# Kernel optimization log

Hardware: AMD Instinct MI355X
Metric: run time of the kernel (lower is better)

Reference implementation:

```python
import jax, jax.numpy as jnp
import numpy as np

EPS_NORM = 1e-12   # F.normalize clamp
EPS_DIV = 1e-6


def _l2_normalize(x):
    n = jnp.linalg.norm(x, axis=-1, keepdims=True)
    return x / jnp.maximum(n, EPS_NORM)


def _sync_stats(video, audio):
    # video, audio: [B, L]
    L = video.shape[-1]
    v = _l2_normalize(video)
    a = _l2_normalize(audio)
    # full cross-correlation per sample -> [B, 2L-1] (same as np.correlate mode='full')
    corr = jax.vmap(lambda vi, ai: jnp.correlate(vi, ai, mode='full'))(v, a)
    peak_idx = jnp.argmax(corr, axis=-1)                     # [B]
    delay = (peak_idx - (L - 1)).astype(jnp.float32)         # center = (2L-1)//2 = L-1
    vnorm = jnp.linalg.norm(v, axis=-1)
    anorm = jnp.linalg.norm(a, axis=-1)
    corr_strength = jnp.max(corr, axis=-1) / (vnorm * anorm + EPS_DIV)
    corr_variance = jnp.std(corr, axis=-1)
    video_energy = jnp.sum(v * v, axis=-1)
    audio_energy = jnp.sum(a * a, axis=-1)
    energy_ratio = video_energy / (audio_energy + EPS_DIV)
    d = v - a
    # |mean(exp(i d))| without complex dtype
    phase_coherence = jnp.sqrt(jnp.mean(jnp.cos(d), axis=-1) ** 2
                               + jnp.mean(jnp.sin(d), axis=-1) ** 2)
    consistency = 1.0 / (1.0 + jnp.abs(delay))
    return jnp.stack([delay / 10.0, corr_strength, corr_variance,
                      energy_ratio, phase_coherence, consistency], axis=-1)  # [B, 6]


def setup_inputs() -> dict:
    key = jax.random.key(0)
    k1, k2, k3, k4, k5, k6 = jax.random.split(key, 6)
    B, L, F = 65536, 128, 32
    return {
        'video_features': jax.random.normal(k1, (B, L), dtype=jnp.float32),
        'audio_features': jax.random.normal(k2, (B, L), dtype=jnp.float32),
        'W1': jax.random.normal(k3, (6, 16), dtype=jnp.float32) * 0.3,
        'b1': jax.random.normal(k4, (16,), dtype=jnp.float32) * 0.1,
        'W2': jax.random.normal(k5, (16, F), dtype=jnp.float32) * 0.2,
        'b2': jax.random.normal(k6, (F,), dtype=jnp.float32) * 0.1,
    }


def reference(video_features, audio_features, W1, b1, W2, b2):
    s = _sync_stats(video_features, audio_features)          # [B, 6]
    h = jax.nn.relu(s @ W1 + b1)                              # [B, 16]
    return h @ W2 + b2                                        # [B, 32]
```

## Files before the change

kernel.cpp:

```cpp
#include <hip/hip_runtime.h>

#define NEG_BIG (-3.0e38f)

__device__ __forceinline__ int swz(int s) { return s ^ ((s >> 3) & 7); }

__global__ __launch_bounds__(256) void avsync_kernel(
    const float* __restrict__ video, const float* __restrict__ audio,
    const float* __restrict__ W1, const float* __restrict__ b1,
    const float* __restrict__ W2, const float* __restrict__ b2,
    float* __restrict__ out) {
  __shared__ float lds[4][2][512];

  const int tid  = threadIdx.x;
  const int wid  = tid >> 6;
  const int lane = tid & 63;
  const int half = lane >> 5;
  const int m    = lane & 31;
  const int b    = (int)blockIdx.x * 8 + wid * 2 + half;

  float* ap  = &lds[wid][half][0];
  float* vl  = &lds[wid][half][384];
  char*  apc = reinterpret_cast<char*>(ap);

  const float4 vr = *reinterpret_cast<const float4*>(video + (size_t)b * 128 + 4 * m);
  const float4 ar = *reinterpret_cast<const float4*>(audio + (size_t)b * 128 + 4 * m);

  float4 z4; z4.x = z4.y = z4.z = z4.w = 0.0f;
  *reinterpret_cast<float4*>(apc + (swz(m)      << 4)) = z4;
  *reinterpret_cast<float4*>(apc + (swz(32 + m) << 4)) = ar;
  *reinterpret_cast<float4*>(apc + (swz(64 + m) << 4)) = z4;
  reinterpret_cast<float4*>(vl)[m] = vr;

  float pv = vr.x * vr.x + vr.y * vr.y + vr.z * vr.z + vr.w * vr.w;
  float pa = ar.x * ar.x + ar.y * ar.y + ar.z * ar.z + ar.w * ar.w;
#pragma unroll
  for (int off = 1; off < 32; off <<= 1) {
    pv += __shfl_xor(pv, off, 32);
    pa += __shfl_xor(pa, off, 32);
  }
  const float nv = sqrtf(pv);
  const float na = sqrtf(pa);
  const float iv = 1.0f / fmaxf(nv, 1e-12f);
  const float ia = 1.0f / fmaxf(na, 1e-12f);

  const float d0 = vr.x * iv - ar.x * ia;
  const float d1 = vr.y * iv - ar.y * ia;
  const float d2 = vr.z * iv - ar.z * ia;
  const float d3 = vr.w * iv - ar.w * ia;
  float sc = __cosf(d0) + __cosf(d1) + __cosf(d2) + __cosf(d3);
  float ss = __sinf(d0) + __sinf(d1) + __sinf(d2) + __sinf(d3);
#pragma unroll
  for (int off = 1; off < 32; off <<= 1) {
    sc += __shfl_xor(sc, off, 32);
    ss += __shfl_xor(ss, off, 32);
  }

  float W[12];
  {
    const float4 t0 = *reinterpret_cast<const float4*>(apc + (swz(2 * m)     << 4));
    const float4 t1 = *reinterpret_cast<const float4*>(apc + (swz(2 * m + 1) << 4));
    const float4 t2 = *reinterpret_cast<const float4*>(apc + (swz(2 * m + 2) << 4));
    W[0] = t0.x; W[1] = t0.y; W[2]  = t0.z; W[3]  = t0.w;
    W[4] = t1.x; W[5] = t1.y; W[6]  = t1.z; W[7]  = t1.w;
    W[8] = t2.x; W[9] = t2.y; W[10] = t2.z; W[11] = t2.w;
  }
  const float4* vlp = reinterpret_cast<const float4*>(vl);
  float acc[8] = {0.f, 0.f, 0.f, 0.f, 0.f, 0.f, 0.f, 0.f};
#pragma unroll
  for (int c = 0; c < 32; ++c) {
    const float4 v4 = vlp[c];
#pragma unroll
    for (int q = 0; q < 8; ++q) {
      acc[q] = fmaf(v4.x, W[7 - q],  acc[q]);
      acc[q] = fmaf(v4.y, W[8 - q],  acc[q]);
      acc[q] = fmaf(v4.z, W[9 - q],  acc[q]);
      acc[q] = fmaf(v4.w, W[10 - q], acc[q]);
    }
    if (c < 31) {
      const float4 tn = *reinterpret_cast<const float4*>(apc + (swz(2 * m + 3 + c) << 4));
#pragma unroll
      for (int k = 0; k < 8; ++k) W[k] = W[k + 4];
      W[8] = tn.x; W[9] = tn.y; W[10] = tn.z; W[11] = tn.w;
    }
  }

  const int sh0 = 248 - 8 * m;
  float sum = 0.f, ssq = 0.f, mx = NEG_BIG;
  int mi = 0;
#pragma unroll
  for (int q = 0; q < 8; ++q) {
    const int sh = sh0 + q;
    const bool realLag = (sh < 255);
    const float cv = acc[q];
    const float cs = realLag ? cv : 0.f;
    sum += cs;
    ssq += cs * cs;
    const float cm = realLag ? cv : NEG_BIG;
    if (cm > mx) { mx = cm; mi = sh; }
  }
#pragma unroll
  for (int off = 1; off < 32; off <<= 1) {
    const float ov = __shfl_xor(mx, off, 32);
    const int   oi = __shfl_xor(mi, off, 32);
    if (ov > mx || (ov == mx && oi < mi)) { mx = ov; mi = oi; }
    sum += __shfl_xor(sum, off, 32);
    ssq += __shfl_xor(ssq, off, 32);
  }

  const float s = iv * ia;
  const float delay = (float)mi - 127.0f;
  const float rv = nv / fmaxf(nv, 1e-12f);
  const float ra = na / fmaxf(na, 1e-12f);
  const float cstr = (mx * s) / (rv * ra + 1e-6f);
  const float mean_r = sum * (1.0f / 255.0f);
  const float var_r  = fmaxf(ssq * (1.0f / 255.0f) - mean_r * mean_r, 0.0f);
  const float cstd = s * sqrtf(var_r);
  const float ve = rv * rv, ae = ra * ra;
  const float er = ve / (ae + 1e-6f);
  const float mc = sc * (1.0f / 128.0f), ms = ss * (1.0f / 128.0f);
  const float pc = sqrtf(mc * mc + ms * ms);
  const float cons = 1.0f / (1.0f + fabsf(delay));

  const float s0 = delay * 0.1f;
  const float s1 = cstr;
  const float s2 = cstd;
  const float s3 = er;
  const float s4 = pc;
  const float s5 = cons;

  float h[16];
#pragma unroll
  for (int k = 0; k < 16; ++k) {
    float acch = b1[k];
    acch = fmaf(s0, W1[0 * 16 + k], acch);
    acch = fmaf(s1, W1[1 * 16 + k], acch);
    acch = fmaf(s2, W1[2 * 16 + k], acch);
    acch = fmaf(s3, W1[3 * 16 + k], acch);
    acch = fmaf(s4, W1[4 * 16 + k], acch);
    acch = fmaf(s5, W1[5 * 16 + k], acch);
    h[k] = fmaxf(acch, 0.0f);
  }
  float o = b2[m];
#pragma unroll
  for (int k = 0; k < 16; ++k) o = fmaf(h[k], W2[k * 32 + m], o);
  out[(size_t)b * 32 + m] = o;
}

extern "C" void kernel_launch(void* const* d_in, const int* in_sizes, int n_in,
                              void* d_out, int out_size, void* d_ws, size_t ws_size,
                              hipStream_t stream) {
  const float* video = (const float*)d_in[0];
  const float* audio = (const float*)d_in[1];
  const float* W1 = (const float*)d_in[2];
  const float* b1 = (const float*)d_in[3];
  const float* W2 = (const float*)d_in[4];
  const float* b2 = (const float*)d_in[5];
  float* out = (float*)d_out;

  const int B = in_sizes[0] / 128;
  const int blocks = B / 8;
  avsync_kernel<<<blocks, 256, 0, stream>>>(video, audio, W1, b1, W2, b2, out);
}
```

Before: 88.67 us.

## Restructure cross-correlation lag mapping with rotating register window and unswizzled LDS

Each lane now computes two groups of four lags (4m..4m+3 and 128+4m..) instead of eight contiguous lags. The shifted audio windows are read as float4 from an unswizzled, padded LDS buffer using a three-register rotation, with loads prefetched one chunk ahead. The change also sets launch_bounds to 8 blocks per unit and drops the XOR swizzle. The aim is to cut register shuffling and LDS address arithmetic and to raise occupancy, at the risk of LDS bank conflicts from the unswizzled reads and register pressure under the new bound.

```diff
diff --git a/kernel.cpp b/kernel.cpp
--- a/kernel.cpp
+++ b/kernel.cpp
@@ -2,14 +2,12 @@
 
 #define NEG_BIG (-3.0e38f)
 
-__device__ __forceinline__ int swz(int s) { return s ^ ((s >> 3) & 7); }
-
-__global__ __launch_bounds__(256) void avsync_kernel(
+__global__ __launch_bounds__(256, 8) void avsync_kernel(
     const float* __restrict__ video, const float* __restrict__ audio,
     const float* __restrict__ W1, const float* __restrict__ b1,
     const float* __restrict__ W2, const float* __restrict__ b2,
     float* __restrict__ out) {
-  __shared__ float lds[4][2][512];
+  __shared__ float lds[4][2][544];
 
   const int tid  = threadIdx.x;
   const int wid  = tid >> 6;
@@ -18,21 +16,21 @@
   const int m    = lane & 31;
   const int b    = (int)blockIdx.x * 8 + wid * 2 + half;
 
-  float* ap  = &lds[wid][half][0];
-  float* vl  = &lds[wid][half][384];
-  char*  apc = reinterpret_cast<char*>(ap);
-
-  const float4 vr = *reinterpret_cast<const float4*>(video + (size_t)b * 128 + 4 * m);
-  const float4 ar = *reinterpret_cast<const float4*>(audio + (size_t)b * 128 + 4 * m);
+  float* hbase = &lds[wid][half][0];
+
+  const float4 v4 = *reinterpret_cast<const float4*>(video + (size_t)b * 128 + 4 * m);
+  const float4 a4 = *reinterpret_cast<const float4*>(audio + (size_t)b * 128 + 4 * m);
 
   float4 z4; z4.x = z4.y = z4.z = z4.w = 0.0f;
-  *reinterpret_cast<float4*>(apc + (swz(m)      << 4)) = z4;
-  *reinterpret_cast<float4*>(apc + (swz(32 + m) << 4)) = ar;
-  *reinterpret_cast<float4*>(apc + (swz(64 + m) << 4)) = z4;
-  reinterpret_cast<float4*>(vl)[m] = vr;
-
-  float pv = vr.x * vr.x + vr.y * vr.y + vr.z * vr.z + vr.w * vr.w;
-  float pa = ar.x * ar.x + ar.y * ar.y + ar.z * ar.z + ar.w * ar.w;
+  float4* sl = reinterpret_cast<float4*>(hbase);
+  sl[m]      = z4;
+  sl[64 + m] = z4;
+  if (m < 2) sl[96 + m] = z4;
+  sl[32 + m] = a4;
+  *reinterpret_cast<float4*>(hbase + 392 + 4 * m) = v4;
+
+  float pv = v4.x * v4.x + v4.y * v4.y + v4.z * v4.z + v4.w * v4.w;
+  float pa = a4.x * a4.x + a4.y * a4.y + a4.z * a4.z + a4.w * a4.w;
 #pragma unroll
   for (int off = 1; off < 32; off <<= 1) {
     pv += __shfl_xor(pv, off, 32);
@@ -43,10 +41,10 @@
   const float iv = 1.0f / fmaxf(nv, 1e-12f);
   const float ia = 1.0f / fmaxf(na, 1e-12f);
 
-  const float d0 = vr.x * iv - ar.x * ia;
-  const float d1 = vr.y * iv - ar.y * ia;
-  const float d2 = vr.z * iv - ar.z * ia;
-  const float d3 = vr.w * iv - ar.w * ia;
+  const float d0 = v4.x * iv - a4.x * ia;
+  const float d1 = v4.y * iv - a4.y * ia;
+  const float d2 = v4.z * iv - a4.z * ia;
+  const float d3 = v4.w * iv - a4.w * ia;
   float sc = __cosf(d0) + __cosf(d1) + __cosf(d2) + __cosf(d3);
   float ss = __sinf(d0) + __sinf(d1) + __sinf(d2) + __sinf(d3);
 #pragma unroll
@@ -55,49 +53,97 @@
     ss += __shfl_xor(ss, off, 32);
   }
 
-  float W[12];
-  {
-    const float4 t0 = *reinterpret_cast<const float4*>(apc + (swz(2 * m)     << 4));
-    const float4 t1 = *reinterpret_cast<const float4*>(apc + (swz(2 * m + 1) << 4));
-    const float4 t2 = *reinterpret_cast<const float4*>(apc + (swz(2 * m + 2) << 4));
-    W[0] = t0.x; W[1] = t0.y; W[2]  = t0.z; W[3]  = t0.w;
-    W[4] = t1.x; W[5] = t1.y; W[6]  = t1.z; W[7]  = t1.w;
-    W[8] = t2.x; W[9] = t2.y; W[10] = t2.z; W[11] = t2.w;
-  }
-  const float4* vlp = reinterpret_cast<const float4*>(vl);
-  float acc[8] = {0.f, 0.f, 0.f, 0.f, 0.f, 0.f, 0.f, 0.f};
-#pragma unroll
-  for (int c = 0; c < 32; ++c) {
-    const float4 v4 = vlp[c];
-#pragma unroll
-    for (int q = 0; q < 8; ++q) {
-      acc[q] = fmaf(v4.x, W[7 - q],  acc[q]);
-      acc[q] = fmaf(v4.y, W[8 - q],  acc[q]);
-      acc[q] = fmaf(v4.z, W[9 - q],  acc[q]);
-      acc[q] = fmaf(v4.w, W[10 - q], acc[q]);
-    }
-    if (c < 31) {
-      const float4 tn = *reinterpret_cast<const float4*>(apc + (swz(2 * m + 3 + c) << 4));
-#pragma unroll
-      for (int k = 0; k < 8; ++k) W[k] = W[k + 4];
-      W[8] = tn.x; W[9] = tn.y; W[10] = tn.z; W[11] = tn.w;
-    }
-  }
-
-  const int sh0 = 248 - 8 * m;
-  float sum = 0.f, ssq = 0.f, mx = NEG_BIG;
-  int mi = 0;
-#pragma unroll
-  for (int q = 0; q < 8; ++q) {
-    const int sh = sh0 + q;
-    const bool realLag = (sh < 255);
-    const float cv = acc[q];
-    const float cs = realLag ? cv : 0.f;
-    sum += cs;
-    ssq += cs * cs;
-    const float cm = realLag ? cv : NEG_BIG;
-    if (cm > mx) { mx = cm; mi = sh; }
-  }
+  const float4* wbase0 = reinterpret_cast<const float4*>(hbase) + (63 - m);
+  const float4* wbase1 = reinterpret_cast<const float4*>(hbase) + (31 - m);
+  const float4* vbase  = reinterpret_cast<const float4*>(hbase + 392);
+
+  float acc00 = 0.f, acc01 = 0.f, acc02 = 0.f, acc03 = 0.f;
+  float acc10 = 0.f, acc11 = 0.f, acc12 = 0.f, acc13 = 0.f;
+
+  float4 wr0 = wbase0[0], wr1 = wbase0[1], wr2;
+  float4 ws0 = wbase1[0], ws1 = wbase1[1], ws2;
+  float4 wv0 = vbase[0], wv1;
+
+#define CHUNK(c, A0, B0, C0, A1, B1, C1, VA, VB)                               \
+  do {                                                                         \
+    if ((c) < 31) {                                                            \
+      (C0) = wbase0[(c) + 2];                                                  \
+      (C1) = wbase1[(c) + 2];                                                  \
+      (VB) = vbase[(c) + 1];                                                   \
+    }                                                                          \
+    acc00 = fmaf((VA).x, (A0).w, acc00); acc00 = fmaf((VA).y, (B0).x, acc00);  \
+    acc00 = fmaf((VA).z, (B0).y, acc00); acc00 = fmaf((VA).w, (B0).z, acc00);  \
+    acc01 = fmaf((VA).x, (A0).z, acc01); acc01 = fmaf((VA).y, (A0).w, acc01);  \
+    acc01 = fmaf((VA).z, (B0).x, acc01); acc01 = fmaf((VA).w, (B0).y, acc01);  \
+    acc02 = fmaf((VA).x, (A0).y, acc02); acc02 = fmaf((VA).y, (A0).z, acc02);  \
+    acc02 = fmaf((VA).z, (A0).w, acc02); acc02 = fmaf((VA).w, (B0).x, acc02);  \
+    acc03 = fmaf((VA).x, (A0).x, acc03); acc03 = fmaf((VA).y, (A0).y, acc03);  \
+    acc03 = fmaf((VA).z, (A0).z, acc03); acc03 = fmaf((VA).w, (A0).w, acc03);  \
+    acc10 = fmaf((VA).x, (A1).w, acc10); acc10 = fmaf((VA).y, (B1).x, acc10);  \
+    acc10 = fmaf((VA).z, (B1).y, acc10); acc10 = fmaf((VA).w, (B1).z, acc10);  \
+    acc11 = fmaf((VA).x, (A1).z, acc11); acc11 = fmaf((VA).y, (A1).w, acc11);  \
+    acc11 = fmaf((VA).z, (B1).x, acc11); acc11 = fmaf((VA).w, (B1).y, acc11);  \
+    acc12 = fmaf((VA).x, (A1).y, acc12); acc12 = fmaf((VA).y, (A1).z, acc12);  \
+    acc12 = fmaf((VA).z, (A1).w, acc12); acc12 = fmaf((VA).w, (B1).x, acc12);  \
+    acc13 = fmaf((VA).x, (A1).x, acc13); acc13 = fmaf((VA).y, (A1).y, acc13);  \
+    acc13 = fmaf((VA).z, (A1).z, acc13); acc13 = fmaf((VA).w, (A1).w, acc13);  \
+  } while (0)
+
+  CHUNK( 0, wr0, wr1, wr2, ws0, ws1, ws2, wv0, wv1);
+  CHUNK( 1, wr1, wr2, wr0, ws1, ws2, ws0, wv1, wv0);
+  CHUNK( 2, wr2, wr0, wr1, ws2, ws0, ws1, wv0, wv1);
+  CHUNK( 3, wr0, wr1, wr2, ws0, ws1, ws2, wv1, wv0);
+  CHUNK( 4, wr1, wr2, wr0, ws1, ws2, ws0, wv0, wv1);
+  CHUNK( 5, wr2, wr0, wr1, ws2, ws0, ws1, wv1, wv0);
+  CHUNK( 6, wr0, wr1, wr2, ws0, ws1, ws2, wv0, wv1);
+  CHUNK( 7, wr1, wr2, wr0, ws1, ws2, ws0, wv1, wv0);
+  CHUNK( 8, wr2, wr0, wr1, ws2, ws0, ws1, wv0, wv1);
+  CHUNK( 9, wr0, wr1, wr2, ws0, ws1, ws2, wv1, wv0);
+  CHUNK(10, wr1, wr2, wr0, ws1, ws2, ws0, wv0, wv1);
+  CHUNK(11, wr2, wr0, wr1, ws2, ws0, ws1, wv1, wv0);
+  CHUNK(12, wr0, wr1, wr2, ws0, ws1, ws2, wv0, wv1);
+  CHUNK(13, wr1, wr2, wr0, ws1, ws2, ws0, wv1, wv0);
+  CHUNK(14, wr2, wr0, wr1, ws2, ws0, ws1, wv0, wv1);
+  CHUNK(15, wr0, wr1, wr2, ws0, ws1, ws2, wv1, wv0);
+  CHUNK(16, wr1, wr2, wr0, ws1, ws2, ws0, wv0, wv1);
+  CHUNK(17, wr2, wr0, wr1, ws2, ws0, ws1, wv1, wv0);
+  CHUNK(18, wr0, wr1, wr2, ws0, ws1, ws2, wv0, wv1);
+  CHUNK(19, wr1, wr2, wr0, ws1, ws2, ws0, wv1, wv0);
+  CHUNK(20, wr2, wr0, wr1, ws2, ws0, ws1, wv0, wv1);
+  CHUNK(21, wr0, wr1, wr2, ws0, ws1, ws2, wv1, wv0);
+  CHUNK(22, wr1, wr2, wr0, ws1, ws2, ws0, wv0, wv1);
+  CHUNK(23, wr2, wr0, wr1, ws2, ws0, ws1, wv1, wv0);
+  CHUNK(24, wr0, wr1, wr2, ws0, ws1, ws2, wv0, wv1);
+  CHUNK(25, wr1, wr2, wr0, ws1, ws2, ws0, wv1, wv0);
+  CHUNK(26, wr2, wr0, wr1, ws2, ws0, ws1, wv0, wv1);
+  CHUNK(27, wr0, wr1, wr2, ws0, ws1, ws2, wv1, wv0);
+  CHUNK(28, wr1, wr2, wr0, ws1, ws2, ws0, wv0, wv1);
+  CHUNK(29, wr2, wr0, wr1, ws2, ws0, ws1, wv1, wv0);
+  CHUNK(30, wr0, wr1, wr2, ws0, ws1, ws2, wv0, wv1);
+  CHUNK(31, wr1, wr2, wr0, ws1, ws2, ws0, wv1, wv0);
+#undef CHUNK
+
+  float sum, ssq, mx; int mi;
+  mx = acc00; mi = 4 * m;
+  sum = acc00; ssq = acc00 * acc00;
+  if (acc01 > mx) { mx = acc01; mi = 4 * m + 1; }
+  sum += acc01; ssq = fmaf(acc01, acc01, ssq);
+  if (acc02 > mx) { mx = acc02; mi = 4 * m + 2; }
+  sum += acc02; ssq = fmaf(acc02, acc02, ssq);
+  if (acc03 > mx) { mx = acc03; mi = 4 * m + 3; }
+  sum += acc03; ssq = fmaf(acc03, acc03, ssq);
+  if (acc10 > mx) { mx = acc10; mi = 128 + 4 * m; }
+  sum += acc10; ssq = fmaf(acc10, acc10, ssq);
+  if (acc11 > mx) { mx = acc11; mi = 128 + 4 * m + 1; }
+  sum += acc11; ssq = fmaf(acc11, acc11, ssq);
+  if (acc12 > mx) { mx = acc12; mi = 128 + 4 * m + 2; }
+  sum += acc12; ssq = fmaf(acc12, acc12, ssq);
+  const bool real13 = (m < 31);
+  const float c13 = real13 ? acc13 : NEG_BIG;
+  if (c13 > mx) { mx = c13; mi = 128 + 4 * m + 3; }
+  const float c13s = real13 ? acc13 : 0.f;
+  sum += c13s; ssq = fmaf(c13s, c13s, ssq);
+
 #pragma unroll
   for (int off = 1; off < 32; off <<= 1) {
     const float ov = __shfl_xor(mx, off, 32);
```

After: 113.4 us. +27.9%, slower.
